# Optimization experiments

Measured on AMD Instinct MI355X. Metric: run time of the kernel, lower is better.

Reference implementation:

```python
import jax, jax.numpy as jnp
import numpy as np

E = 1024
H = 16
N, S, T = 4, 2048, 2048


def setup_inputs() -> dict:
    key = jax.random.key(0)
    ks = jax.random.split(key, 11)
    scale = 1.0 / np.sqrt(E)
    inp = {
        "query": jax.random.normal(ks[0], (N, S, E), jnp.float32),
        "key": jax.random.normal(ks[1], (N, T, E), jnp.float32),
        "value": jax.random.normal(ks[2], (N, T, E), jnp.float32),
        "Wq": jax.random.normal(ks[3], (E, E), jnp.float32) * scale,
        "bq": jax.random.normal(ks[4], (E,), jnp.float32) * 0.01,
        "Wk": jax.random.normal(ks[5], (E, E), jnp.float32) * scale,
        "bk": jax.random.normal(ks[6], (E,), jnp.float32) * 0.01,
        "Wv": jax.random.normal(ks[7], (E, E), jnp.float32) * scale,
        "bv": jax.random.normal(ks[8], (E,), jnp.float32) * 0.01,
        "Wp": jax.random.normal(ks[9], (E, E), jnp.float32) * scale,
        "bp": jax.random.normal(ks[10], (E,), jnp.float32) * 0.01,
    }
    return inp


def reference(query, key, value, Wq, bq, Wk, bk, Wv, bv, Wp, bp):
    n, s, e = query.shape
    t = value.shape[1]
    hd = e // H
    # Linear projections (torch Linear: x @ W^T + b), split into heads -> [N,H,S,hd]
    Q = (query @ Wq.T + bq).reshape(n, s, H, hd).transpose(0, 2, 1, 3)
    K = (key @ Wk.T + bk).reshape(n, t, H, hd).transpose(0, 2, 1, 3)
    V = (value @ Wv.T + bv).reshape(n, t, H, hd).transpose(0, 2, 1, 3)
    scale = 1.0 / jnp.sqrt(jnp.asarray(hd, Q.dtype))
    attn = jnp.einsum("nhsd,nhtd->nhst", Q, K) * scale  # [N,H,S,T]
    A = jax.nn.softmax(attn, axis=-1)
    Y = jnp.einsum("nhst,nhtd->nhsd", A, V)  # [N,H,S,hd]
    Y = Y.transpose(0, 2, 1, 3).reshape(n, s, e)
    return Y @ Wp.T + bp
```

## Files before the change

kernel.cpp:

```cpp
#include <hip/hip_runtime.h>
#include <hip/hip_bf16.h>
#include <stdint.h>


#define E_DIM 1024
#define H_NUM 16
#define HD 64
#define NB 4
#define SEQ 2048
#define NTOK (NB * SEQ)

typedef __bf16 bf16x8 __attribute__((ext_vector_type(8)));
typedef float f32x4 __attribute__((ext_vector_type(4)));
typedef float f32x16 __attribute__((ext_vector_type(16)));
typedef unsigned short u16;

#define MFMA16(a, b, c) __builtin_amdgcn_mfma_f32_16x16x32_bf16(a, b, c, 0, 0, 0)
#define MFMA32(a, b, c) __builtin_amdgcn_mfma_f32_32x32x16_bf16(a, b, c, 0, 0, 0)

#define VMCNT(n) asm volatile("s_waitcnt vmcnt(" #n ")" ::: "memory")
#define BAR() __builtin_amdgcn_s_barrier()
#define PRIO1() __builtin_amdgcn_s_setprio(1)
#define PRIO0() __builtin_amdgcn_s_setprio(0)

__device__ __forceinline__ u16 f2bf(float f) {
  unsigned int u = __builtin_bit_cast(unsigned int, f);
  unsigned int r = (u + 0x7FFFu + ((u >> 16) & 1u)) >> 16;
  return (u16)r;
}

__device__ __forceinline__ float fexp2(float x) {
  return __builtin_amdgcn_exp2f(x);
}

__device__ __forceinline__ void gload_lds16(const void* g, void* l) {
  __builtin_amdgcn_global_load_lds((const __attribute__((address_space(1))) void*)g,
                                   (__attribute__((address_space(3))) void*)l,
                                   16, 0, 0);
}

__device__ __forceinline__ unsigned cvtpk(float lo, float hi2) {
  unsigned w;
  asm("v_cvt_pk_bf16_f32 %0, %1, %2" : "=v"(w) : "v"(lo), "v"(hi2));
  return w;
}
__device__ __forceinline__ void plswap(unsigned& a, unsigned& b) {
  asm("v_permlane32_swap_b32 %0, %1" : "+v"(a), "+v"(b));
}

template <int B0>
__device__ __forceinline__ bf16x8 packpa(const f32x16& pe) {
  unsigned wa = cvtpk(pe[B0 + 0], pe[B0 + 1]);
  unsigned wb = cvtpk(pe[B0 + 4], pe[B0 + 5]);
  unsigned wc2 = cvtpk(pe[B0 + 2], pe[B0 + 3]);
  unsigned wd = cvtpk(pe[B0 + 6], pe[B0 + 7]);
  plswap(wa, wb);
  plswap(wc2, wd);
  union { unsigned u[4]; bf16x8 v; } pa;
  pa.u[0] = wa; pa.u[1] = wc2; pa.u[2] = wb; pa.u[3] = wd;
  return pa.v;
}

__global__ __launch_bounds__(256) void cvt7(const float* __restrict__ s0,
                                            const float* __restrict__ s1,
                                            const float* __restrict__ s2,
                                            const float* __restrict__ s3,
                                            const float* __restrict__ s4,
                                            const float* __restrict__ s5,
                                            const float* __restrict__ s6,
                                            u16* d0, u16* d1, u16* d2, u16* d3,
                                            u16* d4, u16* d5, u16* d6,
                                            int nbig, int nsmall) {
  const int t = blockIdx.y;
  const float* in;
  u16* out;
  int n4;
  switch (t) {
    case 0: in = s0; out = d0; n4 = nbig; break;
    case 1: in = s1; out = d1; n4 = nbig; break;
    case 2: in = s2; out = d2; n4 = nbig; break;
    case 3: in = s3; out = d3; n4 = nsmall; break;
    case 4: in = s4; out = d4; n4 = nsmall; break;
    case 5: in = s5; out = d5; n4 = nsmall; break;
    default: in = s6; out = d6; n4 = nsmall; break;
  }
  int idx = blockIdx.x * 256 + threadIdx.x;
  int stride = gridDim.x * 256;
  for (int i = idx; i < n4; i += stride) {
    float4 v = ((const float4*)in)[i];
    ushort4 o;
    o.x = f2bf(v.x); o.y = f2bf(v.y); o.z = f2bf(v.z); o.w = f2bf(v.w);
    ((ushort4*)out)[i] = o;
  }
}

__device__ __forceinline__ void rdA(bf16x8 (&af)[4][2], const char* pA, int off,
                                    int cs0, int cs1) {
#pragma unroll
  for (int mi = 0; mi < 4; mi++) {
    af[mi][0] = *(const bf16x8*)(pA + off + mi * 2048 + cs0);
    af[mi][1] = *(const bf16x8*)(pA + off + mi * 2048 + cs1);
  }
}
__device__ __forceinline__ void rdB(bf16x8 (&bfr)[2][2], const char* pB, int off,
                                    int cs0, int cs1) {
#pragma unroll
  for (int nj = 0; nj < 2; nj++) {
    bfr[nj][0] = *(const bf16x8*)(pB + off + nj * 2048 + cs0);
    bfr[nj][1] = *(const bf16x8*)(pB + off + nj * 2048 + cs1);
  }
}
template <int MI0, int NJ0>
__device__ __forceinline__ void mm16(f32x4 (&acc)[8][4], bf16x8 (&af)[4][2],
                                     bf16x8 (&bfr)[2][2]) {
#pragma unroll
  for (int kk = 0; kk < 2; kk++)
#pragma unroll
    for (int mi = 0; mi < 4; mi++)
#pragma unroll
      for (int nj = 0; nj < 2; nj++)
        acc[MI0 + mi][NJ0 + nj] = MFMA16(af[mi][kk], bfr[nj][kk], acc[MI0 + mi][NJ0 + nj]);
}

__global__ void __launch_bounds__(512, 2) gemm_qkv8(
    const u16* __restrict__ qb, const u16* __restrict__ kb, const u16* __restrict__ vb,
    const u16* __restrict__ Wcat, const float* __restrict__ bq,
    const float* __restrict__ bk, const float* __restrict__ bv,
    u16* __restrict__ Qp, u16* __restrict__ Kp, u16* __restrict__ Vt, float qscale) {
  extern __shared__ char LDS[];
  const int tid = threadIdx.x;
  const int w = tid >> 6, l = tid & 63;
  const int lr = l & 15, lg = l >> 4;
  const int wr = w >> 2, wc2 = w & 3;
  const int m0 = blockIdx.x * 256;
  const int n0g = blockIdx.y * 256;
  const int z = blockIdx.y >> 2;
  const u16* A = (z == 0) ? qb : (z == 1) ? kb : vb;

  const int swz = (lr & 7) << 4;
  const int cs0 = (lg << 4) ^ swz;
  const int cs1 = ((lg << 4) + 64) ^ swz;
  const char* pA = LDS + (wr * 16384 + lr * 128);
  const char* pB = LDS + (65536 + (wc2 >> 1) * 16384 + ((wc2 & 1) * 64 + lr) * 128);

  const int sr0 = tid >> 3;
  const int sc = (((tid & 7) * 16) ^ ((sr0 & 7) << 4)) >> 1;
  const u16* aS[2];
  const u16* bS[2];
#pragma unroll
  for (int ld = 0; ld < 2; ld++) {
    aS[ld] = A + (size_t)(m0 + ld * 64 + sr0) * E_DIM + sc;
    bS[ld] = Wcat + (size_t)(n0g + ld * 64 + sr0) * E_DIM + sc;
  }

#define STG_A(h, kt)                                                                   \
  do {                                                                                 \
    const int _b = (kt) & 1;                                                           \
    gload_lds16(aS[0] + (h) * 131072 + (size_t)(kt) * 64,                              \
                LDS + _b * 32768 + (h) * 16384 + w * 1024);                            \
    gload_lds16(aS[1] + (h) * 131072 + (size_t)(kt) * 64,                              \
                LDS + _b * 32768 + (h) * 16384 + w * 1024 + 8192);                     \
  } while (0)
#define STG_B(h, kt)                                                                   \
  do {                                                                                 \
    const int _b = (kt) & 1;                                                           \
    gload_lds16(bS[0] + (h) * 131072 + (size_t)(kt) * 64,                              \
                LDS + 65536 + _b * 32768 + (h) * 16384 + w * 1024);                    \
    gload_lds16(bS[1] + (h) * 131072 + (size_t)(kt) * 64,                              \
                LDS + 65536 + _b * 32768 + (h) * 16384 + w * 1024 + 8192);             \
  } while (0)

  f32x4 acc[8][4] = {};
  bf16x8 af[4][2], bfr[2][2];

#define FRAME(T, LAST)                                                                 \
  do {                                                                                 \
    rdA(af, pA, 0, cs0, cs1); rdB(bfr, pB, 0, cs0, cs1);                               \
    STG_B(0, (T) + 1);                                                                 \
    BAR(); PRIO1(); mm16<0, 0>(acc, af, bfr); PRIO0(); BAR();                          \
    rdB(bfr, pB, 4096, cs0, cs1);                                                      \
    STG_B(1, (T) + 1);                                                                 \
    BAR(); PRIO1(); mm16<0, 2>(acc, af, bfr); PRIO0(); BAR();                          \
    rdA(af, pA, 8192, cs0, cs1);                                                       \
    STG_A(1, (T) + 1);                                                                 \
    BAR(); PRIO1(); mm16<4, 2>(acc, af, bfr); PRIO0(); BAR();                          \
    rdB(bfr, pB, 0, cs0, cs1);                                                         \
    if (!(LAST)) { STG_A(0, (T) + 2); VMCNT(2); } else { VMCNT(0); }                   \
    BAR(); PRIO1(); mm16<4, 0>(acc, af, bfr); PRIO0(); BAR();                          \
    rdA(af, pA, 32768, cs0, cs1); rdB(bfr, pB, 32768, cs0, cs1);                       \
    if (!(LAST)) STG_B(0, (T) + 2);                                                    \
    BAR(); PRIO1(); mm16<0, 0>(acc, af, bfr); PRIO0(); BAR();                          \
    rdB(bfr, pB, 32768 + 4096, cs0, cs1);                                              \
    if (!(LAST)) STG_B(1, (T) + 2);                                                    \
    BAR(); PRIO1(); mm16<0, 2>(acc, af, bfr); PRIO0(); BAR();                          \
    rdA(af, pA, 32768 + 8192, cs0, cs1);                                               \
    if (!(LAST)) STG_A(1, (T) + 2);                                                    \
    BAR(); PRIO1(); mm16<4, 2>(acc, af, bfr); PRIO0(); BAR();                          \
    rdB(bfr, pB, 32768, cs0, cs1);                                                     \
    if (!(LAST)) { STG_A(0, (T) + 3); VMCNT(2); }                                      \
    BAR(); PRIO1(); mm16<4, 0>(acc, af, bfr); PRIO0(); BAR();                          \
  } while (0)

  STG_A(0, 0); STG_A(1, 0); STG_B(0, 0); STG_B(1, 0); STG_A(0, 1);
  VMCNT(2);
  BAR();

#pragma unroll 1
  for (int T = 0; T < 14; T += 2) FRAME(T, false);
  FRAME(14, true);

  const float* bias = (z == 0) ? bq : (z == 1) ? bk : bv;
  const float osc = (z == 0) ? qscale : 1.0f;
#pragma unroll
  for (int mi = 0; mi < 8; mi++) {
#pragma unroll
    for (int nj = 0; nj < 4; nj++) {
      const int colm = (n0g + wc2 * 64 + nj * 16 + lr) & 1023;
      const float bvv = bias[colm];
      const int row0 = m0 + wr * 128 + mi * 16 + lg * 4;
      if (z == 2) {
        const int nb = row0 >> 11, t = row0 & (SEQ - 1);
        const int hh = colm >> 6, d = colm & 63;
        ushort4 o;
        o.x = f2bf(acc[mi][nj][0] + bvv);
        o.y = f2bf(acc[mi][nj][1] + bvv);
        o.z = f2bf(acc[mi][nj][2] + bvv);
        o.w = f2bf(acc[mi][nj][3] + bvv);
        *(ushort4*)&Vt[(((size_t)((nb * H_NUM + hh) * HD + d)) << 11) + t] = o;
      } else {
        u16* Cb = (z == 0) ? Qp : Kp;
#pragma unroll
        for (int ri = 0; ri < 4; ri++)
          Cb[(size_t)(row0 + ri) * E_DIM + colm] = f2bf((acc[mi][nj][ri] + bvv) * osc);
      }
    }
  }
#undef FRAME
#undef STG_A
#undef STG_B
}

__global__ __launch_bounds__(256) void gemm_proj(const u16* __restrict__ A,
                                                 const u16* __restrict__ W,
                                                 const float* __restrict__ bias,
                                                 float* __restrict__ Cout) {
  __shared__ u16 As[2][128 * 32];
  __shared__ u16 Bs[2][128 * 32];
  const int tid = threadIdx.x;
  const int w = tid >> 6, l = tid & 63;
  const int lg = l >> 4, lr = l & 15;
  const int m0 = blockIdx.y * 128, n0 = blockIdx.x * 128;
  const int wr = (w >> 1) * 64, wc = (w & 1) * 64;
  f32x4 acc[4][4] = {};
  const int qa0 = w, qa1 = 4 + w;
  const int rowA0 = qa0 * 16 + (l >> 2), rowA1 = qa1 * 16 + (l >> 2);
  const int colA = (l & 3) * 8;
  const u16* aptr0 = A + (size_t)(m0 + rowA0) * E_DIM + colA;
  const u16* aptr1 = A + (size_t)(m0 + rowA1) * E_DIM + colA;
  const u16* bptr0 = W + (size_t)(n0 + rowA0) * E_DIM + colA;
  const u16* bptr1 = W + (size_t)(n0 + rowA1) * E_DIM + colA;

#define GSTAGE(B, k0)                                   \
  do {                                                  \
    gload_lds16(aptr0 + (k0), &As[B][qa0 * 512]);       \
    gload_lds16(aptr1 + (k0), &As[B][qa1 * 512]);       \
    gload_lds16(bptr0 + (k0), &Bs[B][qa0 * 512]);       \
    gload_lds16(bptr1 + (k0), &Bs[B][qa1 * 512]);       \
  } while (0)
#define GBODY(B)                                                          \
  do {                                                                    \
    bf16x8 af[4], bfr[4];                                                 \
    _Pragma("unroll") for (int mi = 0; mi < 4; mi++)                      \
      af[mi] = *(const bf16x8*)&As[B][(wr + mi * 16 + lr) * 32 + lg * 8]; \
    _Pragma("unroll") for (int nj = 0; nj < 4; nj++)                      \
      bfr[nj] = *(const bf16x8*)&Bs[B][(wc + nj * 16 + lr) * 32 + lg * 8];\
    _Pragma("unroll") for (int mi = 0; mi < 4; mi++)                      \
      _Pragma("unroll") for (int nj = 0; nj < 4; nj++)                    \
        acc[mi][nj] = MFMA16(af[mi], bfr[nj], acc[mi][nj]);               \
  } while (0)

  GSTAGE(0, 0);
  __syncthreads();
#pragma unroll 1
  for (int k0 = 0; k0 < E_DIM; k0 += 64) {
    GSTAGE(1, k0 + 32);
    GBODY(0);
    __syncthreads();
    if (k0 + 64 < E_DIM) GSTAGE(0, k0 + 64);
    GBODY(1);
    __syncthreads();
  }
#pragma unroll
  for (int mi = 0; mi < 4; mi++) {
#pragma unroll
    for (int nj = 0; nj < 4; nj++) {
      const int col = n0 + wc + nj * 16 + lr;
      const float bv = bias[col];
      const int row0 = m0 + wr + mi * 16 + lg * 4;
#pragma unroll
      for (int ri = 0; ri < 4; ri++)
        Cout[(size_t)(row0 + ri) * E_DIM + col] = acc[mi][nj][ri] + bv;
    }
  }
#undef GSTAGE
#undef GBODY
}

__global__ __launch_bounds__(256, 2) void attn_kernel(const u16* __restrict__ Qp,
                                                      const u16* __restrict__ Kp,
                                                      const u16* __restrict__ Vt,
                                                      u16* __restrict__ Yb) {
  __shared__ u16 Ks[2][64 * 64];
  __shared__ u16 Vs[2][64 * 64];
  const int h = blockIdx.x, qt = blockIdx.y, n = blockIdx.z;
  const int tid = threadIdx.x;
  const int w = tid >> 6, l = tid & 63;
  const int c = l & 31, hi = l >> 5;
  const int q0 = qt * 256 + w * 64;

  bf16x8 qfA[4], qfB[4];
  {
    const u16* qrowA = Qp + (size_t)(n * SEQ + q0 + c) * E_DIM + h * HD + hi * 8;
    const u16* qrowB = qrowA + 32 * E_DIM;
#pragma unroll
    for (int ks = 0; ks < 4; ks++) {
      qfA[ks] = *(const bf16x8*)(qrowA + ks * 16);
      qfB[ks] = *(const bf16x8*)(qrowB + ks * 16);
    }
  }

  f32x16 yA0 = {}, yA1 = {}, yB0 = {}, yB1 = {};
  float lrA = 0.f, lrB = 0.f;

  int lo[4];
#pragma unroll
  for (int ks = 0; ks < 4; ks++)
    lo[ks] = c * 128 + ((ks * 32 + hi * 16) ^ ((c & 7) << 4));

  const int sr = l >> 3;
  const int sc = ((l & 7) ^ sr) * 8;
  const u16* kgb[2];
  const u16* vgb[2];
#pragma unroll
  for (int g = 0; g < 2; g++) {
    const int row_ = (w << 4) + (g << 3) + sr;
    kgb[g] = Kp + (size_t)(n * SEQ + row_) * E_DIM + h * HD + sc;
    vgb[g] = Vt + ((size_t)((n * H_NUM + h) * HD + row_)) * SEQ + sc;
  }

#define STAGE(B, t0)                                                    \
  do {                                                                  \
    gload_lds16(kgb[0] + (size_t)(t0) * E_DIM, &Ks[B][(w << 10)]);      \
    gload_lds16(kgb[1] + (size_t)(t0) * E_DIM, &Ks[B][(w << 10) + 512]);\
    gload_lds16(vgb[0] + (t0), &Vs[B][(w << 10)]);                      \
    gload_lds16(vgb[1] + (t0), &Vs[B][(w << 10) + 512]);                \
  } while (0)

#define TILE_BODY(B)                                                           \
  do {                                                                         \
    const char* kb = (const char*)Ks[B];                                       \
    const char* vb = (const char*)Vs[B];                                       \
    f32x16 sA0 = {}, sA1 = {}, sB0 = {}, sB1 = {};                             \
    PRIO1();                                                                   \
    _Pragma("unroll") for (int ks = 0; ks < 4; ks++) {                         \
      bf16x8 ka0 = *(const bf16x8*)(kb + lo[ks]);                              \
      bf16x8 ka1 = *(const bf16x8*)(kb + lo[ks] + 4096);                       \
      sA0 = MFMA32(ka0, qfA[ks], sA0);                                         \
      sA1 = MFMA32(ka1, qfA[ks], sA1);                                         \
      sB0 = MFMA32(ka0, qfB[ks], sB0);                                         \
      sB1 = MFMA32(ka1, qfB[ks], sB1);                                         \
    }                                                                          \
    PRIO0();                                                                   \
    float pa0 = 0.f, pa1 = 0.f, pb0 = 0.f, pb1 = 0.f;                          \
    _Pragma("unroll") for (int r = 0; r < 8; r++) {                            \
      sA0[r] = fexp2(sA0[r]);         pa0 += sA0[r];                           \
      sA0[r + 8] = fexp2(sA0[r + 8]); pa1 += sA0[r + 8];                       \
      sA1[r] = fexp2(sA1[r]);         pa0 += sA1[r];                           \
      sA1[r + 8] = fexp2(sA1[r + 8]); pa1 += sA1[r + 8];                       \
      sB0[r] = fexp2(sB0[r]);         pb0 += sB0[r];                           \
      sB0[r + 8] = fexp2(sB0[r + 8]); pb1 += sB0[r + 8];                       \
      sB1[r] = fexp2(sB1[r]);         pb0 += sB1[r];                           \
      sB1[r + 8] = fexp2(sB1[r + 8]); pb1 += sB1[r + 8];                       \
    }                                                                          \
    lrA += pa0 + pa1;                                                          \
    lrB += pb0 + pb1;                                                          \
    PRIO1();                                                                   \
    _Pragma("unroll") for (int ks = 0; ks < 4; ks++) {                         \
      const f32x16& peA = (ks < 2) ? sA0 : sA1;                                \
      const f32x16& peB = (ks < 2) ? sB0 : sB1;                                \
      bf16x8 paA, paB;                                                         \
      if (ks & 1) { paA = packpa<8>(peA); paB = packpa<8>(peB); }              \
      else        { paA = packpa<0>(peA); paB = packpa<0>(peB); }              \
      bf16x8 va0 = *(const bf16x8*)(vb + lo[ks]);                              \
      bf16x8 va1 = *(const bf16x8*)(vb + lo[ks] + 4096);                       \
      yA0 = MFMA32(va0, paA, yA0);                                             \
      yA1 = MFMA32(va1, paA, yA1);                                             \
      yB0 = MFMA32(va0, paB, yB0);                                             \
      yB1 = MFMA32(va1, paB, yB1);                                             \
    }                                                                          \
    PRIO0();                                                                   \
  } while (0)

  STAGE(0, 0);
  __syncthreads();

#pragma unroll 1
  for (int it = 0; it < SEQ / 64; it += 2) {
    STAGE(1, (it + 1) * 64);
    TILE_BODY(0);
    __syncthreads();
    if (it + 2 < SEQ / 64) STAGE(0, (it + 2) * 64);
    TILE_BODY(1);
    __syncthreads();
  }

  lrA += __shfl_xor(lrA, 32, 64);
  lrB += __shfl_xor(lrB, 32, 64);
  const float invA = 1.f / lrA;
  const float invB = 1.f / lrB;
  u16* orowA = Yb + (size_t)(n * SEQ + q0 + c) * E_DIM + h * HD;
  u16* orowB = orowA + (size_t)32 * E_DIM;
#pragma unroll
  for (int df = 0; df < 2; df++) {
    const f32x16 ya = df ? yA1 : yA0;
    const f32x16 yb2 = df ? yB1 : yB0;
#pragma unroll
    for (int g = 0; g < 4; g++) {
      ushort4 oA, oB;
      oA.x = f2bf(ya[g * 4 + 0] * invA);
      oA.y = f2bf(ya[g * 4 + 1] * invA);
      oA.z = f2bf(ya[g * 4 + 2] * invA);
      oA.w = f2bf(ya[g * 4 + 3] * invA);
      oB.x = f2bf(yb2[g * 4 + 0] * invB);
      oB.y = f2bf(yb2[g * 4 + 1] * invB);
      oB.z = f2bf(yb2[g * 4 + 2] * invB);
      oB.w = f2bf(yb2[g * 4 + 3] * invB);
      *(ushort4*)(orowA + df * 32 + g * 8 + hi * 4) = oA;
      *(ushort4*)(orowB + df * 32 + g * 8 + hi * 4) = oB;
    }
  }
#undef STAGE
#undef TILE_BODY
}

extern "C" void kernel_launch(void* const* d_in, const int* in_sizes, int n_in,
                              void* d_out, int out_size, void* d_ws, size_t ws_size,
                              hipStream_t stream) {
  const float* query = (const float*)d_in[0];
  const float* key   = (const float*)d_in[1];
  const float* value = (const float*)d_in[2];
  const float* Wq = (const float*)d_in[3];
  const float* bq = (const float*)d_in[4];
  const float* Wk = (const float*)d_in[5];
  const float* bk = (const float*)d_in[6];
  const float* Wv = (const float*)d_in[7];
  const float* bv = (const float*)d_in[8];
  const float* Wp = (const float*)d_in[9];
  const float* bp = (const float*)d_in[10];

  const size_t TOK_E = (size_t)NTOK * E_DIM;
  const size_t W_E = (size_t)E_DIM * E_DIM;

  u16* ws = (u16*)d_ws;
  u16* qb  = ws;
  u16* kb  = qb + TOK_E;
  u16* vb  = kb + TOK_E;
  u16* wqb = vb + TOK_E;
  u16* wkb = wqb + W_E;
  u16* wvb = wkb + W_E;
  u16* wpb = wvb + W_E;
  u16* Qp  = wpb + W_E;
  u16* Kp  = Qp + TOK_E;
  u16* Vtb = Kp + TOK_E;
  u16* Yb  = Vtb + TOK_E;

  cvt7<<<dim3(1024, 7), 256, 0, stream>>>(query, key, value, Wq, Wk, Wv, Wp,
                                          qb, kb, vb, wqb, wkb, wvb, wpb,
                                          (int)(TOK_E / 4), (int)(W_E / 4));

  const float sc2 = 0.125f * 1.44269504088896f;

  hipFuncSetAttribute((const void*)gemm_qkv8,
                      hipFuncAttributeMaxDynamicSharedMemorySize, 131072);
  gemm_qkv8<<<dim3(NTOK / 256, 3072 / 256), 512, 131072, stream>>>(
      qb, kb, vb, wqb, bq, bk, bv, Qp, Kp, Vtb, sc2);

  attn_kernel<<<dim3(H_NUM, SEQ / 256, NB), 256, 0, stream>>>(Qp, Kp, Vtb, Yb);

  gemm_proj<<<dim3(E_DIM / 128, NTOK / 128), 256, 0, stream>>>(Yb, wpb, bp, (float*)d_out);
}
```

Baseline: 193.0 us.

## Split key sequence across two wave groups per attention block and merge via LDS

Doubles the attention block to 512 threads, with two 4-wave groups each processing half of the key/value sequence into separate LDS buffers. The partial output accumulators and softmax denominators are combined through shared memory before normalization and the store. The aim is more resident waves per CU to hide latency, at the cost of an LDS reduction epilogue with extra barriers. The tighter launch bound also pressures the register budget.

After: 667.0 us. 246% more time.

```diff
diff --git a/kernel.cpp b/kernel.cpp
--- a/kernel.cpp
+++ b/kernel.cpp
@@ -306,17 +306,20 @@
 #undef GBODY
 }
 
-__global__ __launch_bounds__(256, 2) void attn_kernel(const u16* __restrict__ Qp,
+__global__ __launch_bounds__(512, 4) void attn_kernel(const u16* __restrict__ Qp,
                                                       const u16* __restrict__ Kp,
                                                       const u16* __restrict__ Vt,
                                                       u16* __restrict__ Yb) {
-  __shared__ u16 Ks[2][64 * 64];
-  __shared__ u16 Vs[2][64 * 64];
+  __shared__ char SMEM[65536];
   const int h = blockIdx.x, qt = blockIdx.y, n = blockIdx.z;
   const int tid = threadIdx.x;
   const int w = tid >> 6, l = tid & 63;
+  const int g = w >> 2, wl = w & 3;
   const int c = l & 31, hi = l >> 5;
-  const int q0 = qt * 256 + w * 64;
+  const int q0 = qt * 256 + wl * 64;
+
+  char* const kbuf = SMEM + g * 32768;
+  char* const vbuf = SMEM + g * 32768 + 16384;
 
   bf16x8 qfA[4], qfB[4];
   {
@@ -342,24 +345,24 @@
   const u16* kgb[2];
   const u16* vgb[2];
 #pragma unroll
-  for (int g = 0; g < 2; g++) {
-    const int row_ = (w << 4) + (g << 3) + sr;
-    kgb[g] = Kp + (size_t)(n * SEQ + row_) * E_DIM + h * HD + sc;
-    vgb[g] = Vt + ((size_t)((n * H_NUM + h) * HD + row_)) * SEQ + sc;
-  }
-
-#define STAGE(B, t0)                                                    \
-  do {                                                                  \
-    gload_lds16(kgb[0] + (size_t)(t0) * E_DIM, &Ks[B][(w << 10)]);      \
-    gload_lds16(kgb[1] + (size_t)(t0) * E_DIM, &Ks[B][(w << 10) + 512]);\
-    gload_lds16(vgb[0] + (t0), &Vs[B][(w << 10)]);                      \
-    gload_lds16(vgb[1] + (t0), &Vs[B][(w << 10) + 512]);                \
+  for (int g2 = 0; g2 < 2; g2++) {
+    const int row_ = (wl << 4) + (g2 << 3) + sr;
+    kgb[g2] = Kp + (size_t)(n * SEQ + g * 1024 + row_) * E_DIM + h * HD + sc;
+    vgb[g2] = Vt + ((size_t)((n * H_NUM + h) * HD + row_)) * SEQ + g * 1024 + sc;
+  }
+
+#define STAGE(B, t0)                                                        \
+  do {                                                                      \
+    gload_lds16(kgb[0] + (size_t)(t0) * E_DIM, kbuf + (B) * 8192 + wl * 2048);        \
+    gload_lds16(kgb[1] + (size_t)(t0) * E_DIM, kbuf + (B) * 8192 + wl * 2048 + 1024); \
+    gload_lds16(vgb[0] + (t0), vbuf + (B) * 8192 + wl * 2048);              \
+    gload_lds16(vgb[1] + (t0), vbuf + (B) * 8192 + wl * 2048 + 1024);       \
   } while (0)
 
 #define TILE_BODY(B)                                                           \
   do {                                                                         \
-    const char* kb = (const char*)Ks[B];                                       \
-    const char* vb = (const char*)Vs[B];                                       \
+    const char* kb = kbuf + (B) * 8192;                                        \
+    const char* vb = vbuf + (B) * 8192;                                        \
     f32x16 sA0 = {}, sA1 = {}, sB0 = {}, sB1 = {};                             \
     PRIO1();                                                                   \
     _Pragma("unroll") for (int ks = 0; ks < 4; ks++) {                         \
@@ -405,38 +408,80 @@
   __syncthreads();
 
 #pragma unroll 1
-  for (int it = 0; it < SEQ / 64; it += 2) {
+  for (int it = 0; it < 16; it += 2) {
     STAGE(1, (it + 1) * 64);
     TILE_BODY(0);
     __syncthreads();
-    if (it + 2 < SEQ / 64) STAGE(0, (it + 2) * 64);
+    if (it + 2 < 16) STAGE(0, (it + 2) * 64);
     TILE_BODY(1);
     __syncthreads();
   }
 
   lrA += __shfl_xor(lrA, 32, 64);
   lrB += __shfl_xor(lrB, 32, 64);
-  const float invA = 1.f / lrA;
-  const float invB = 1.f / lrB;
-  u16* orowA = Yb + (size_t)(n * SEQ + q0 + c) * E_DIM + h * HD;
-  u16* orowB = orowA + (size_t)32 * E_DIM;
-#pragma unroll
-  for (int df = 0; df < 2; df++) {
-    const f32x16 ya = df ? yA1 : yA0;
-    const f32x16 yb2 = df ? yB1 : yB0;
-#pragma unroll
-    for (int g = 0; g < 4; g++) {
-      ushort4 oA, oB;
-      oA.x = f2bf(ya[g * 4 + 0] * invA);
-      oA.y = f2bf(ya[g * 4 + 1] * invA);
-      oA.z = f2bf(ya[g * 4 + 2] * invA);
-      oA.w = f2bf(ya[g * 4 + 3] * invA);
-      oB.x = f2bf(yb2[g * 4 + 0] * invB);
-      oB.y = f2bf(yb2[g * 4 + 1] * invB);
-      oB.z = f2bf(yb2[g * 4 + 2] * invB);
-      oB.w = f2bf(yb2[g * 4 + 3] * invB);
-      *(ushort4*)(orowA + df * 32 + g * 8 + hi * 4) = oA;
-      *(ushort4*)(orowB + df * 32 + g * 8 + hi * 4) = oB;
+  float* const reg = (float*)SMEM + wl * 2112;
+  u16* const orowA = Yb + (size_t)(n * SEQ + q0 + c) * E_DIM + h * HD;
+  u16* const orowB = orowA + (size_t)32 * E_DIM;
+
+  if (g == 1) {
+#pragma unroll
+    for (int r = 0; r < 16; r++) {
+      reg[l + 64 * r] = yA0[r];
+      reg[l + 64 * (16 + r)] = yA1[r];
+    }
+    reg[l + 2048] = lrA;
+  }
+  __syncthreads();
+  if (g == 0) {
+#pragma unroll
+    for (int r = 0; r < 16; r++) {
+      yA0[r] += reg[l + 64 * r];
+      yA1[r] += reg[l + 64 * (16 + r)];
+    }
+    const float invA = 1.f / (lrA + reg[l + 2048]);
+#pragma unroll
+    for (int df = 0; df < 2; df++) {
+      const f32x16 ya = df ? yA1 : yA0;
+#pragma unroll
+      for (int gg = 0; gg < 4; gg++) {
+        ushort4 o;
+        o.x = f2bf(ya[gg * 4 + 0] * invA);
+        o.y = f2bf(ya[gg * 4 + 1] * invA);
+        o.z = f2bf(ya[gg * 4 + 2] * invA);
+        o.w = f2bf(ya[gg * 4 + 3] * invA);
+        *(ushort4*)(orowA + df * 32 + gg * 8 + hi * 4) = o;
+      }
+    }
+  }
+  __syncthreads();
+  if (g == 1) {
+#pragma unroll
+    for (int r = 0; r < 16; r++) {
+      reg[l + 64 * r] = yB0[r];
+      reg[l + 64 * (16 + r)] = yB1[r];
+    }
+    reg[l + 2048] = lrB;
+  }
+  __syncthreads();
+  if (g == 0) {
+#pragma unroll
+    for (int r = 0; r < 16; r++) {
+      yB0[r] += reg[l + 64 * r];
+      yB1[r] += reg[l + 64 * (16 + r)];
+    }
+    const float invB = 1.f / (lrB + reg[l + 2048]);
+#pragma unroll
+    for (int df = 0; df < 2; df++) {
+      const f32x16 yb2 = df ? yB1 : yB0;
+#pragma unroll
+      for (int gg = 0; gg < 4; gg++) {
+        ushort4 o;
+        o.x = f2bf(yb2[gg * 4 + 0] * invB);
+        o.y = f2bf(yb2[gg * 4 + 1] * invB);
+        o.z = f2bf(yb2[gg * 4 + 2] * invB);
+        o.w = f2bf(yb2[gg * 4 + 3] * invB);
+        *(ushort4*)(orowB + df * 32 + gg * 8 + hi * 4) = o;
+      }
     }
   }
 #undef STAGE
@@ -485,7 +530,7 @@
   gemm_qkv8<<<dim3(NTOK / 256, 3072 / 256), 512, 131072, stream>>>(
       qb, kb, vb, wqb, bq, bk, bv, Qp, Kp, Vtb, sc2);
 
-  attn_kernel<<<dim3(H_NUM, SEQ / 256, NB), 256, 0, stream>>>(Qp, Kp, Vtb, Yb);
+  attn_kernel<<<dim3(H_NUM, SEQ / 256, NB), 512, 0, stream>>>(Qp, Kp, Vtb, Yb);
 
   gemm_proj<<<dim3(E_DIM / 128, NTOK / 128), 256, 0, stream>>>(Yb, wpb, bp, (float*)d_out);
 }
```
